# Optimization experiments

Hardware: AMD Instinct MI355X
Metric: run time of the kernel (lower is better)

## Reference

```python
import jax, jax.numpy as jnp
import numpy as np

D_MODEL = 256
N_LAYERS = 4
D_STATE = 16
D_CONV = 4
D_INNER = 2 * D_MODEL          # expand=2
DT_RANK = (D_MODEL + 15) // 16  # 'auto' -> ceil(d_model/16) = 16
NUM_CLASSES = 10
BATCH = 4
HW = 32


def setup_inputs() -> dict:
    key = jax.random.key(0)
    ks = jax.random.split(key, 16)
    std = 0.02
    inp = {}
    inp["x"] = jax.random.normal(ks[0], (BATCH, 3, HW, HW), dtype=jnp.float32)
    inp["input_proj_w"] = std * jax.random.normal(ks[1], (D_MODEL, 3), dtype=jnp.float32)
    inp["input_proj_b"] = jnp.zeros((D_MODEL,), jnp.float32)
    inp["in_proj_w"] = std * jax.random.normal(ks[2], (N_LAYERS, 2 * D_INNER, D_MODEL), dtype=jnp.float32)
    inp["conv_w"] = std * jax.random.normal(ks[3], (N_LAYERS, D_INNER, D_CONV), dtype=jnp.float32)
    inp["conv_b"] = jnp.zeros((N_LAYERS, D_INNER), jnp.float32)
    inp["x_proj_w"] = std * jax.random.normal(ks[4], (N_LAYERS, DT_RANK + 2 * D_STATE, D_INNER), dtype=jnp.float32)
    inp["dt_proj_w"] = std * jax.random.normal(ks[5], (N_LAYERS, D_INNER, DT_RANK), dtype=jnp.float32)
    # dt bias ~ inverse-softplus of small dt values (Mamba-style init)
    inp["dt_proj_b"] = jnp.log(jnp.expm1(0.01 * jnp.ones((N_LAYERS, D_INNER), jnp.float32)))
    # A_log init: log(1..d_state) per channel (Mamba S4D-real init)
    a = jnp.log(jnp.arange(1, D_STATE + 1, dtype=jnp.float32))
    inp["A_log"] = jnp.broadcast_to(a, (N_LAYERS, D_INNER, D_STATE)).copy()
    inp["D_skip"] = jnp.ones((N_LAYERS, D_INNER), jnp.float32)
    inp["out_proj_w"] = std * jax.random.normal(ks[6], (N_LAYERS, D_MODEL, D_INNER), dtype=jnp.float32)
    inp["ln_w"] = jnp.ones((N_LAYERS, D_MODEL), jnp.float32)
    inp["ln_b"] = jnp.zeros((N_LAYERS, D_MODEL), jnp.float32)
    inp["fn_w"] = jnp.ones((D_MODEL,), jnp.float32)
    inp["fn_b"] = jnp.zeros((D_MODEL,), jnp.float32)
    inp["cls_w"] = std * jax.random.normal(ks[7], (NUM_CLASSES, D_MODEL), dtype=jnp.float32)
    inp["cls_b"] = jnp.zeros((NUM_CLASSES,), jnp.float32)
    return inp


def _layer_norm(x, w, b, eps=1e-5):
    mu = jnp.mean(x, axis=-1, keepdims=True)
    var = jnp.mean(jnp.square(x - mu), axis=-1, keepdims=True)
    return (x - mu) * jax.lax.rsqrt(var + eps) * w + b


def _mamba_block(x, in_w, cw, cb, xp_w, dt_w, dt_b, A_log, D_skip, out_w):
    B_, L, _ = x.shape
    xz = jnp.einsum('bld,ed->ble', x, in_w)            # [B,L,2*Din]
    xh, z = jnp.split(xz, 2, axis=-1)                  # [B,L,Din] each
    # depthwise causal conv1d (kernel D_CONV, left pad D_CONV-1)
    xp = jnp.pad(xh, ((0, 0), (D_CONV - 1, 0), (0, 0)))
    conv = cb + sum(xp[:, k:k + L, :] * cw[:, k] for k in range(D_CONV))
    xh = jax.nn.silu(conv)
    x_dbl = jnp.einsum('bld,ed->ble', xh, xp_w)        # [B,L,dt_rank+2N]
    dt, Bm, Cm = jnp.split(x_dbl, [DT_RANK, DT_RANK + D_STATE], axis=-1)
    delta = jax.nn.softplus(jnp.einsum('blr,dr->bld', dt, dt_w) + dt_b)  # [B,L,Din]
    A = -jnp.exp(A_log)                                # [Din,N]
    deltaA = jnp.exp(delta[..., None] * A)             # [B,L,Din,N]
    deltaBu = delta[..., None] * Bm[:, :, None, :] * xh[..., None]       # [B,L,Din,N]

    def step(h, inputs):
        dA_t, dBu_t, C_t = inputs
        h = dA_t * h + dBu_t                           # [B,Din,N]
        y = jnp.einsum('bdn,bn->bd', h, C_t)
        return h, y

    h0 = jnp.zeros((B_, D_INNER, D_STATE), x.dtype)
    _, ys = jax.lax.scan(step, h0, (deltaA.transpose(1, 0, 2, 3),
                                    deltaBu.transpose(1, 0, 2, 3),
                                    Cm.transpose(1, 0, 2)))
    y = ys.transpose(1, 0, 2) + xh * D_skip            # [B,L,Din]
    y = y * jax.nn.silu(z)
    return jnp.einsum('bld,od->blo', y, out_w)         # [B,L,Dmodel]


def reference(x, input_proj_w, input_proj_b, in_proj_w, conv_w, conv_b,
              x_proj_w, dt_proj_w, dt_proj_b, A_log, D_skip, out_proj_w,
              ln_w, ln_b, fn_w, fn_b, cls_w, cls_b):
    B_ = x.shape[0]
    seq = x.transpose(0, 2, 3, 1).reshape(B_, -1, 3)   # [B, H*W, 3]
    h = jnp.einsum('blc,dc->bld', seq, input_proj_w) + input_proj_b
    for i in range(N_LAYERS):
        res = h
        h = _layer_norm(h, ln_w[i], ln_b[i])
        h = _mamba_block(h, in_proj_w[i], conv_w[i], conv_b[i], x_proj_w[i],
                         dt_proj_w[i], dt_proj_b[i], A_log[i], D_skip[i], out_proj_w[i])
        h = h + res  # dropout is identity (p=0 / eval)
    h = jnp.mean(h, axis=1)                            # [B, Dmodel]
    h = _layer_norm(h, fn_w, fn_b)
    return h @ cls_w.T + cls_b                         # [B, num_classes]
```

## Files before the change

kernel.cpp:

```cpp
#include <hip/hip_runtime.h>
#include <math.h>

#define B_ 4
#define L_ 1024
#define DM 256
#define DIN 512
#define NST 16
#define DTR 16
#define CHK 64
#define CT (L_ / CHK)

typedef short short8 __attribute__((ext_vector_type(8)));
typedef float float4v __attribute__((ext_vector_type(4)));

__device__ __forceinline__ float softplusf(float x) {
    return (x > 20.f) ? x : log1pf(__expf(x));
}
__device__ __forceinline__ float siluf(float x) {
    return x / (1.f + __expf(-x));
}
__device__ __forceinline__ unsigned short f2bf(float f) {
    unsigned int u = __float_as_uint(f);
    u = (u + 0x7fffu + ((u >> 16) & 1u)) >> 16;
    return (unsigned short)u;
}

__device__ __forceinline__ void block_reduce2(float& a, float& q) {
    #pragma unroll
    for (int off = 32; off > 0; off >>= 1) {
        a += __shfl_down(a, off);
        q += __shfl_down(q, off);
    }
    __shared__ float sa[4], sq[4];
    int lane = threadIdx.x & 63, w = threadIdx.x >> 6;
    if (lane == 0) { sa[w] = a; sq[w] = q; }
    __syncthreads();
    a = sa[0] + sa[1] + sa[2] + sa[3];
    q = sq[0] + sq[1] + sq[2] + sq[3];
}

__global__ __launch_bounds__(256) void prologue_kernel(
    const float* __restrict__ inw, int na, const float* __restrict__ xpw, int nb,
    const float* __restrict__ opw, int nc,
    unsigned short* __restrict__ oa, unsigned short* __restrict__ ob,
    unsigned short* __restrict__ oc, int nconv,
    const float* __restrict__ x, const float* __restrict__ ipw,
    const float* __restrict__ ipb, const float* __restrict__ lw0,
    const float* __restrict__ lb0, float* __restrict__ h0,
    unsigned short* __restrict__ ln16)
{
    if ((int)blockIdx.x < nconv) {
        int i = blockIdx.x * 256 + threadIdx.x;
        if (i < na) { oa[i] = f2bf(inw[i]); return; }
        int j = i - na;
        if (j < nb) { ob[j] = f2bf(xpw[j]); return; }
        int k = j - nb;
        if (k < nc) oc[k] = f2bf(opw[k]);
        return;
    }
    int row = blockIdx.x - nconv;
    int l = row & (L_ - 1);
    int b = row >> 10;
    int d = threadIdx.x;
    const float* xb = x + (size_t)b * 3 * L_;
    float x0 = xb[l], x1 = xb[L_ + l], x2 = xb[2 * L_ + l];
    float acc = ipb[d];
    acc = fmaf(x0, ipw[d * 3 + 0], acc);
    acc = fmaf(x1, ipw[d * 3 + 1], acc);
    acc = fmaf(x2, ipw[d * 3 + 2], acc);
    float a = acc, q = acc * acc;
    block_reduce2(a, q);
    float mu = a * (1.f / DM);
    float var = q * (1.f / DM) - mu * mu;
    float rs = rsqrtf(var + 1e-5f);
    h0[(size_t)row * DM + d] = acc;
    ln16[(size_t)row * DM + d] = f2bf((acc - mu) * rs * lw0[d] + lb0[d]);
}

__global__ __launch_bounds__(256) void gemm_bt_bf16(
    const unsigned short* __restrict__ A, const unsigned short* __restrict__ W,
    float* __restrict__ C, int M, int N, int K, int lda)
{
    __shared__ unsigned short As[64][72];
    __shared__ unsigned short Ws[64][72];
    const int tid = threadIdx.x;
    const int wave = tid >> 6;
    const int lane = tid & 63;
    const int m_l = lane & 15;
    const int q = lane >> 4;
    const int m0 = blockIdx.y * 64;
    const int n0 = blockIdx.x * 64;
    const int sr = tid >> 3;
    const int sc = (tid & 7) * 8;

    float4v acc[4];
    #pragma unroll
    for (int j = 0; j < 4; ++j) acc[j] = (float4v)(0.f);

    for (int k0 = 0; k0 < K; k0 += 64) {
        *(short8*)&As[sr][sc]      = *(const short8*)(A + (size_t)(m0 + sr) * lda + k0 + sc);
        *(short8*)&As[sr + 32][sc] = *(const short8*)(A + (size_t)(m0 + sr + 32) * lda + k0 + sc);
        *(short8*)&Ws[sr][sc]      = *(const short8*)(W + (size_t)(n0 + sr) * K + k0 + sc);
        *(short8*)&Ws[sr + 32][sc] = *(const short8*)(W + (size_t)(n0 + sr + 32) * K + k0 + sc);
        __syncthreads();
        #pragma unroll
        for (int kk = 0; kk < 64; kk += 32) {
            short8 a = *(const short8*)&As[wave * 16 + m_l][kk + q * 8];
            #pragma unroll
            for (int j4 = 0; j4 < 4; ++j4) {
                short8 bf = *(const short8*)&Ws[j4 * 16 + m_l][kk + q * 8];
                acc[j4] = __builtin_amdgcn_mfma_f32_16x16x32_bf16(a, bf, acc[j4], 0, 0, 0);
            }
        }
        __syncthreads();
    }
    #pragma unroll
    for (int j4 = 0; j4 < 4; ++j4) {
        int n = n0 + j4 * 16 + m_l;
        #pragma unroll
        for (int reg = 0; reg < 4; ++reg) {
            int m = m0 + wave * 16 + q * 4 + reg;
            C[(size_t)m * N + n] = acc[j4][reg];
        }
    }
}

__global__ __launch_bounds__(512) void conv_xproj_summary(
    const float* __restrict__ xz, const float* __restrict__ cw,
    const float* __restrict__ cb, const unsigned short* __restrict__ W,
    const float* __restrict__ A_log, const float* __restrict__ dt_w,
    const float* __restrict__ dt_b,
    float* __restrict__ dbc, float* __restrict__ S, float* __restrict__ H)
{
    __shared__ unsigned short As[CT][520];
    __shared__ float Dbc[CT][64];
    const int tid = threadIdx.x;
    const int d = tid;
    const int c = blockIdx.x;
    const int b = blockIdx.y;
    const int l0 = c * CT;

    float xcr[CT];
    {
        const float w0 = cw[d * 4 + 0], w1 = cw[d * 4 + 1];
        const float w2 = cw[d * 4 + 2], w3 = cw[d * 4 + 3];
        const float cbv = cb[d];
        const float* xp = xz + ((size_t)(b * L_ + l0)) * (2 * DIN) + d;
        float x0 = 0.f, x1 = 0.f, x2 = 0.f;
        if (l0 >= 3) {
            x0 = xp[(ptrdiff_t)(-3) * (2 * DIN)];
            x1 = xp[(ptrdiff_t)(-2) * (2 * DIN)];
            x2 = xp[(ptrdiff_t)(-1) * (2 * DIN)];
        }
        #pragma unroll
        for (int t = 0; t < CT; ++t) {
            float x3 = xp[(size_t)t * (2 * DIN)];
            float a = fmaf(x0, w0, cbv);
            a = fmaf(x1, w1, a);
            a = fmaf(x2, w2, a);
            a = fmaf(x3, w3, a);
            float v = siluf(a);
            xcr[t] = v;
            As[t][d] = f2bf(v);
            x0 = x1; x1 = x2; x2 = x3;
        }
    }
    __syncthreads();

    {
        const int wave = tid >> 6;
        const int lane = tid & 63;
        const int m_l = lane & 15;
        const int q = lane >> 4;
        if (wave < 3) {
            float4v acc = (float4v)(0.f);
            for (int k0 = 0; k0 < DIN; k0 += 32) {
                short8 a  = *(const short8*)&As[m_l][k0 + q * 8];
                short8 bf = *(const short8*)(W + (size_t)(wave * 16 + m_l) * DIN + k0 + q * 8);
                acc = __builtin_amdgcn_mfma_f32_16x16x32_bf16(a, bf, acc, 0, 0, 0);
            }
            #pragma unroll
            for (int reg = 0; reg < 4; ++reg)
                Dbc[q * 4 + reg][wave * 16 + m_l] = acc[reg];
        }
    }
    __syncthreads();

    for (int i = tid; i < CT * 48; i += 512) {
        int t = i / 48, col = i - t * 48;
        dbc[((size_t)(b * L_ + l0 + t)) * 48 + col] = Dbc[t][col];
    }

    float A[NST], tw[DTR];
    #pragma unroll
    for (int j = 0; j < NST; ++j) A[j] = -__expf(A_log[d * NST + j]);
    #pragma unroll
    for (int r = 0; r < DTR; ++r) tw[r] = dt_w[d * DTR + r];
    const float tb = dt_b[d];
    float h[NST];
    #pragma unroll
    for (int j = 0; j < NST; ++j) h[j] = 0.f;
    float ssum = 0.f;
    #pragma unroll 4
    for (int t = 0; t < CT; ++t) {
        float acc = tb;
        #pragma unroll
        for (int r = 0; r < DTR; ++r) acc = fmaf(Dbc[t][r], tw[r], acc);
        float dlt = softplusf(acc);
        float t0 = dlt * xcr[t];
        ssum += dlt;
        #pragma unroll
        for (int j = 0; j < NST; ++j) {
            float dA = __expf(A[j] * dlt);
            h[j] = fmaf(dA, h[j], t0 * Dbc[t][DTR + j]);
        }
    }
    S[((size_t)b * CHK + c) * DIN + d] = ssum;
    float* Hp = H + (((size_t)b * CHK + c) * NST) * DIN + d;
    #pragma unroll
    for (int j = 0; j < NST; ++j)
        Hp[(size_t)j * DIN] = h[j];
}

__global__ __launch_bounds__(256) void scan_prefix_kernel(
    const float* __restrict__ S, float* __restrict__ H,
    const float* __restrict__ A_log)
{
    int idx = blockIdx.x * 256 + threadIdx.x;
    int d = idx & (DIN - 1);
    int n = (idx >> 9) & (NST - 1);
    int b = idx >> 13;
    float A = -__expf(A_log[d * NST + n]);
    float hprev = 0.f;
    const float* Sp = S + (size_t)b * CHK * DIN + d;
    float* Hp = H + (((size_t)b * CHK) * NST + n) * DIN + d;
    for (int c = 0; c < CHK; ++c) {
        float Hc = Hp[(size_t)c * NST * DIN];
        float Sc = Sp[(size_t)c * DIN];
        Hp[(size_t)c * NST * DIN] = hprev;
        hprev = fmaf(__expf(A * Sc), hprev, Hc);
    }
}

__global__ __launch_bounds__(512) void scan_apply_out(
    const float* __restrict__ dbc, const float* __restrict__ xz,
    const float* __restrict__ cw, const float* __restrict__ cb,
    const float* __restrict__ A_log, const float* __restrict__ dt_w,
    const float* __restrict__ dt_b, const float* __restrict__ Dskip,
    const float* __restrict__ H, const unsigned short* __restrict__ Wout,
    float* __restrict__ hbuf, const float* __restrict__ nlw,
    const float* __restrict__ nlb, unsigned short* __restrict__ ln16,
    float* __restrict__ chunkpartial, int last)
{
    __shared__ unsigned short Ys[CT][520];
    __shared__ float hrow[CT][264];
    const int tid = threadIdx.x;
    const int d = tid;
    const int c = blockIdx.x;
    const int b = blockIdx.y;
    const int l0 = c * CT;

    {
        float A[NST], tw[DTR];
        #pragma unroll
        for (int j = 0; j < NST; ++j) A[j] = -__expf(A_log[d * NST + j]);
        #pragma unroll
        for (int r = 0; r < DTR; ++r) tw[r] = dt_w[d * DTR + r];
        const float tb = dt_b[d];
        const float Dsk = Dskip[d];
        const float* bc = dbc + ((size_t)(b * L_ + l0)) * 48;
        const float* xp = xz  + ((size_t)(b * L_ + l0)) * (2 * DIN) + d;
        const float* zp = xp + DIN;

        const float w0 = cw[d * 4 + 0], w1 = cw[d * 4 + 1];
        const float w2 = cw[d * 4 + 2], w3 = cw[d * 4 + 3];
        const float cbv = cb[d];
        float x0 = 0.f, x1 = 0.f, x2 = 0.f;
        if (l0 >= 3) {
            x0 = xp[(ptrdiff_t)(-3) * (2 * DIN)];
            x1 = xp[(ptrdiff_t)(-2) * (2 * DIN)];
            x2 = xp[(ptrdiff_t)(-1) * (2 * DIN)];
        }

        float h[NST];
        const float* Hp = H + (((size_t)b * CHK + c) * NST) * DIN + d;
        #pragma unroll
        for (int j = 0; j < NST; ++j) h[j] = Hp[(size_t)j * DIN];

        #pragma unroll 4
        for (int t = 0; t < CT; ++t) {
            float x3 = xp[(size_t)t * (2 * DIN)];
            float ca = fmaf(x0, w0, cbv);
            ca = fmaf(x1, w1, ca);
            ca = fmaf(x2, w2, ca);
            ca = fmaf(x3, w3, ca);
            float xcv = siluf(ca);
            x0 = x1; x1 = x2; x2 = x3;

            const float* br = bc + t * 48;
            float acc = tb;
            #pragma unroll
            for (int r = 0; r < DTR; ++r) acc = fmaf(br[r], tw[r], acc);
            float dlt = softplusf(acc);
            float zv  = zp[(size_t)t * (2 * DIN)];
            float t0 = dlt * xcv;
            float p = 0.f;
            #pragma unroll
            for (int j = 0; j < NST; ++j) {
                float dA = __expf(A[j] * dlt);
                h[j] = fmaf(dA, h[j], t0 * br[DTR + j]);
                p = fmaf(h[j], br[DTR + NST + j], p);
            }
            Ys[t][d] = f2bf((p + xcv * Dsk) * siluf(zv));
        }
    }
    __syncthreads();

    {
        const int row = tid >> 5;
        const int col0 = (tid & 31) * 8;
        const float* hg = hbuf + ((size_t)(b * L_ + l0 + row)) * DM + col0;
        *(float4*)&hrow[row][col0]     = *(const float4*)hg;
        *(float4*)&hrow[row][col0 + 4] = *(const float4*)(hg + 4);
    }
    __syncthreads();

    {
        const int wave = tid >> 6;
        const int lane = tid & 63;
        const int m_l = lane & 15;
        const int q = lane >> 4;
        #pragma unroll
        for (int nt = 0; nt < 2; ++nt) {
            const int n0 = (wave * 2 + nt) * 16;
            float4v acc;
            #pragma unroll
            for (int reg = 0; reg < 4; ++reg)
                acc[reg] = hrow[q * 4 + reg][n0 + m_l];
            for (int k0 = 0; k0 < DIN; k0 += 32) {
                short8 a = *(const short8*)&Ys[m_l][k0 + q * 8];
                short8 w = *(const short8*)(Wout + (size_t)(n0 + m_l) * DIN + k0 + q * 8);
                acc = __builtin_amdgcn_mfma_f32_16x16x32_bf16(a, w, acc, 0, 0, 0);
            }
            #pragma unroll
            for (int reg = 0; reg < 4; ++reg)
                hrow[q * 4 + reg][n0 + m_l] = acc[reg];
        }
    }
    __syncthreads();

    if (!last) {
        const int row = tid >> 5;
        const int c32 = tid & 31;
        const int col0 = c32 * 8;
        float v[8];
        float s = 0.f, qq = 0.f;
        #pragma unroll
        for (int i = 0; i < 8; ++i) {
            v[i] = hrow[row][col0 + i];
            s += v[i];
            qq += v[i] * v[i];
        }
        s += __shfl_xor(s, 1);  qq += __shfl_xor(qq, 1);
        s += __shfl_xor(s, 2);  qq += __shfl_xor(qq, 2);
        s += __shfl_xor(s, 4);  qq += __shfl_xor(qq, 4);
        s += __shfl_xor(s, 8);  qq += __shfl_xor(qq, 8);
        s += __shfl_xor(s, 16); qq += __shfl_xor(qq, 16);
        float mu = s * (1.f / DM);
        float var = qq * (1.f / DM) - mu * mu;
        float rs = rsqrtf(var + 1e-5f);
        float* hg = hbuf + ((size_t)(b * L_ + l0 + row)) * DM + col0;
        *(float4*)hg       = make_float4(v[0], v[1], v[2], v[3]);
        *(float4*)(hg + 4) = make_float4(v[4], v[5], v[6], v[7]);
        unsigned short* lo = ln16 + ((size_t)(b * L_ + l0 + row)) * DM + col0;
        #pragma unroll
        for (int i = 0; i < 8; ++i)
            lo[i] = f2bf((v[i] - mu) * rs * nlw[col0 + i] + nlb[col0 + i]);
    } else {
        if (tid < DM) {
            float s = 0.f;
            #pragma unroll
            for (int t = 0; t < CT; ++t) s += hrow[t][tid];
            chunkpartial[((size_t)(b * CHK + c)) * DM + tid] = s;
        }
    }
}

__global__ __launch_bounds__(256) void head_final_kernel(
    const float* __restrict__ chunkpartial, const float* __restrict__ fn_w,
    const float* __restrict__ fn_b, const float* __restrict__ cls_w,
    const float* __restrict__ cls_b, float* __restrict__ out)
{
    int b = blockIdx.x, t = threadIdx.x;
    const float* pp = chunkpartial + (size_t)b * CHK * DM + t;
    float s = 0.f;
    #pragma unroll 8
    for (int c = 0; c < CHK; ++c) s += pp[(size_t)c * DM];
    s *= (1.f / L_);
    float a = s, q = s * s;
    block_reduce2(a, q);
    float mu = a * (1.f / DM);
    float var = q * (1.f / DM) - mu * mu;
    float v = (s - mu) * rsqrtf(var + 1e-5f) * fn_w[t] + fn_b[t];
    __shared__ float pooled[DM];
    pooled[t] = v;
    __syncthreads();
    if (t < 10) {
        float acc = cls_b[t];
        for (int d2 = 0; d2 < DM; ++d2)
            acc = fmaf(pooled[d2], cls_w[t * DM + d2], acc);
        out[b * 10 + t] = acc;
    }
}

extern "C" void kernel_launch(void* const* d_in, const int* in_sizes, int n_in,
                              void* d_out, int out_size, void* d_ws, size_t ws_size,
                              hipStream_t stream)
{
    const float* x    = (const float*)d_in[0];
    const float* ipw  = (const float*)d_in[1];
    const float* ipb  = (const float*)d_in[2];
    const float* inw  = (const float*)d_in[3];
    const float* cw   = (const float*)d_in[4];
    const float* cb   = (const float*)d_in[5];
    const float* xpw  = (const float*)d_in[6];
    const float* dtw  = (const float*)d_in[7];
    const float* dtb  = (const float*)d_in[8];
    const float* alog = (const float*)d_in[9];
    const float* dsk  = (const float*)d_in[10];
    const float* opw  = (const float*)d_in[11];
    const float* lnw  = (const float*)d_in[12];
    const float* lnb  = (const float*)d_in[13];
    const float* fnw  = (const float*)d_in[14];
    const float* fnb  = (const float*)d_in[15];
    const float* clw  = (const float*)d_in[16];
    const float* clb  = (const float*)d_in[17];

    float* ws     = (float*)d_ws;
    float* hbuf   = ws;
    float* xzbuf  = hbuf   + (size_t)B_ * L_ * DM;
    float* dbcbuf = xzbuf  + (size_t)B_ * L_ * 2 * DIN;
    float* Sbuf   = dbcbuf + (size_t)B_ * L_ * 48;
    float* Hbuf   = Sbuf   + (size_t)B_ * CHK * DIN;
    float* cpart  = Hbuf   + (size_t)B_ * CHK * NST * DIN;
    float* tail   = cpart  + (size_t)B_ * CHK * DM;
    unsigned short* ln16  = (unsigned short*)tail;
    unsigned short* inw16 = ln16  + (size_t)B_ * L_ * DM;
    unsigned short* xpw16 = inw16 + (size_t)4 * 1024 * DM;
    unsigned short* opw16 = xpw16 + (size_t)4 * 48 * DIN;

    const int BL = B_ * L_;
    const int NIN = 4 * 1024 * DM, NXP = 4 * 48 * DIN, NOP = 4 * DM * DIN;
    const int NCONV = (NIN + NXP + NOP + 255) / 256;

    prologue_kernel<<<NCONV + BL, 256, 0, stream>>>(
        inw, NIN, xpw, NXP, opw, NOP, inw16, xpw16, opw16, NCONV,
        x, ipw, ipb, lnw, lnb, hbuf, ln16);

    for (int i = 0; i < 4; ++i) {
        gemm_bt_bf16<<<dim3(2 * DIN / 64, BL / 64), 256, 0, stream>>>(
            ln16, inw16 + (size_t)i * 1024 * DM, xzbuf, BL, 2 * DIN, DM, DM);
        conv_xproj_summary<<<dim3(CHK, B_), 512, 0, stream>>>(
            xzbuf, cw + i * DIN * 4, cb + i * DIN,
            xpw16 + (size_t)i * 48 * DIN, alog + i * DIN * NST,
            dtw + i * DIN * DTR, dtb + i * DIN, dbcbuf, Sbuf, Hbuf);
        scan_prefix_kernel<<<B_ * NST * DIN / 256, 256, 0, stream>>>(
            Sbuf, Hbuf, alog + i * DIN * NST);
        int last = (i == 3);
        const float* nlw = lnw + (last ? 0 : (i + 1) * DM);
        const float* nlb = lnb + (last ? 0 : (i + 1) * DM);
        scan_apply_out<<<dim3(CHK, B_), 512, 0, stream>>>(
            dbcbuf, xzbuf, cw + i * DIN * 4, cb + i * DIN,
            alog + i * DIN * NST, dtw + i * DIN * DTR, dtb + i * DIN,
            dsk + i * DIN, Hbuf, opw16 + (size_t)i * DM * DIN, hbuf,
            nlw, nlb, ln16, cpart, last);
    }

    head_final_kernel<<<B_, 256, 0, stream>>>(cpart, fnw, fnb, clw, clb,
                                              (float*)d_out);
}
```

Baseline: 385.6 us.

## Fuse in_proj GEMM into conv/xproj kernel and inline chunk-prefix scan into apply

The standalone in_proj GEMM is folded into a per-chunk front kernel. Each block computes its 19-row (16 plus 3 halo) slice of xz via MFMA, keeps the x half in shared memory for the causal conv, and writes conv output and z to separate buffers. The separate scan_prefix kernel is removed: each back-kernel block recomputes its incoming state by looping over all preceding chunk summaries. The change cuts two launches per layer and the xz round trip through memory. In exchange it recomputes halo rows in the GEMM, re-reads in_proj weights from global in every block, and gives later chunks up to 63 serial prefix steps of 16 exps each.

```diff
diff --git a/kernel.cpp b/kernel.cpp
--- a/kernel.cpp
+++ b/kernel.cpp
@@ -77,84 +77,82 @@
     ln16[(size_t)row * DM + d] = f2bf((acc - mu) * rs * lw0[d] + lb0[d]);
 }
 
-__global__ __launch_bounds__(256) void gemm_bt_bf16(
-    const unsigned short* __restrict__ A, const unsigned short* __restrict__ W,
-    float* __restrict__ C, int M, int N, int K, int lda)
+__global__ __launch_bounds__(512) void layer_front(
+    const unsigned short* __restrict__ ln16, const unsigned short* __restrict__ Win,
+    const float* __restrict__ cw, const float* __restrict__ cb,
+    const unsigned short* __restrict__ Wxp, const float* __restrict__ A_log,
+    const float* __restrict__ dt_w, const float* __restrict__ dt_b,
+    float* __restrict__ xcbuf, float* __restrict__ zbuf,
+    float* __restrict__ dbc, float* __restrict__ S, float* __restrict__ H)
 {
-    __shared__ unsigned short As[64][72];
-    __shared__ unsigned short Ws[64][72];
+    __shared__ unsigned short UN[8448];
+    __shared__ float xh[19][528];
+    __shared__ float Dbc[CT][64];
+    unsigned short (*Ln)[264] = (unsigned short (*)[264])UN;
+    unsigned short (*As)[520] = (unsigned short (*)[520])UN;
+
     const int tid = threadIdx.x;
+    const int c = blockIdx.x;
+    const int b = blockIdx.y;
+    const int l0 = c * CT;
     const int wave = tid >> 6;
     const int lane = tid & 63;
     const int m_l = lane & 15;
     const int q = lane >> 4;
-    const int m0 = blockIdx.y * 64;
-    const int n0 = blockIdx.x * 64;
-    const int sr = tid >> 3;
-    const int sc = (tid & 7) * 8;
-
-    float4v acc[4];
-    #pragma unroll
-    for (int j = 0; j < 4; ++j) acc[j] = (float4v)(0.f);
-
-    for (int k0 = 0; k0 < K; k0 += 64) {
-        *(short8*)&As[sr][sc]      = *(const short8*)(A + (size_t)(m0 + sr) * lda + k0 + sc);
-        *(short8*)&As[sr + 32][sc] = *(const short8*)(A + (size_t)(m0 + sr + 32) * lda + k0 + sc);
-        *(short8*)&Ws[sr][sc]      = *(const short8*)(W + (size_t)(n0 + sr) * K + k0 + sc);
-        *(short8*)&Ws[sr + 32][sc] = *(const short8*)(W + (size_t)(n0 + sr + 32) * K + k0 + sc);
-        __syncthreads();
-        #pragma unroll
-        for (int kk = 0; kk < 64; kk += 32) {
-            short8 a = *(const short8*)&As[wave * 16 + m_l][kk + q * 8];
-            #pragma unroll
-            for (int j4 = 0; j4 < 4; ++j4) {
-                short8 bf = *(const short8*)&Ws[j4 * 16 + m_l][kk + q * 8];
-                acc[j4] = __builtin_amdgcn_mfma_f32_16x16x32_bf16(a, bf, acc[j4], 0, 0, 0);
+
+    {
+        const int sr = tid >> 5;
+        const int sc = (tid & 31) * 8;
+        #pragma unroll
+        for (int p = 0; p < 2; ++p) {
+            int row = sr + p * 16;
+            int rr = row > 18 ? 18 : row;
+            int gl = l0 - 3 + rr;
+            if (gl < 0) gl = 0;
+            *(short8*)&Ln[row][sc] =
+                *(const short8*)(ln16 + ((size_t)(b * L_ + gl)) * DM + sc);
+        }
+    }
+    __syncthreads();
+
+    #pragma unroll
+    for (int mt = 0; mt < 2; ++mt) {
+        #pragma unroll
+        for (int nt = 0; nt < 8; ++nt) {
+            const int n0 = wave * 128 + nt * 16;
+            float4v acc = (float4v)(0.f);
+            for (int k0 = 0; k0 < DM; k0 += 32) {
+                short8 a = *(const short8*)&Ln[mt * 16 + m_l][k0 + q * 8];
+                short8 w = *(const short8*)(Win + (size_t)(n0 + m_l) * DM + k0 + q * 8);
+                acc = __builtin_amdgcn_mfma_f32_16x16x32_bf16(a, w, acc, 0, 0, 0);
             }
-        }
-        __syncthreads();
-    }
-    #pragma unroll
-    for (int j4 = 0; j4 < 4; ++j4) {
-        int n = n0 + j4 * 16 + m_l;
-        #pragma unroll
-        for (int reg = 0; reg < 4; ++reg) {
-            int m = m0 + wave * 16 + q * 4 + reg;
-            C[(size_t)m * N + n] = acc[j4][reg];
-        }
-    }
-}
-
-__global__ __launch_bounds__(512) void conv_xproj_summary(
-    const float* __restrict__ xz, const float* __restrict__ cw,
-    const float* __restrict__ cb, const unsigned short* __restrict__ W,
-    const float* __restrict__ A_log, const float* __restrict__ dt_w,
-    const float* __restrict__ dt_b,
-    float* __restrict__ dbc, float* __restrict__ S, float* __restrict__ H)
-{
-    __shared__ unsigned short As[CT][520];
-    __shared__ float Dbc[CT][64];
-    const int tid = threadIdx.x;
+            const int col = n0 + m_l;
+            #pragma unroll
+            for (int reg = 0; reg < 4; ++reg) {
+                int r = mt * 16 + q * 4 + reg;
+                if (r < 19) {
+                    if (col < DIN)
+                        xh[r][col] = acc[reg];
+                    else if (r >= 3)
+                        zbuf[((size_t)(b * L_ + l0 + r - 3)) * DIN + (col - DIN)] = acc[reg];
+                }
+            }
+        }
+    }
+    __syncthreads();
+
     const int d = tid;
-    const int c = blockIdx.x;
-    const int b = blockIdx.y;
-    const int l0 = c * CT;
-
+    if (c == 0) { xh[0][d] = 0.f; xh[1][d] = 0.f; xh[2][d] = 0.f; }
     float xcr[CT];
     {
         const float w0 = cw[d * 4 + 0], w1 = cw[d * 4 + 1];
         const float w2 = cw[d * 4 + 2], w3 = cw[d * 4 + 3];
         const float cbv = cb[d];
-        const float* xp = xz + ((size_t)(b * L_ + l0)) * (2 * DIN) + d;
-        float x0 = 0.f, x1 = 0.f, x2 = 0.f;
-        if (l0 >= 3) {
-            x0 = xp[(ptrdiff_t)(-3) * (2 * DIN)];
-            x1 = xp[(ptrdiff_t)(-2) * (2 * DIN)];
-            x2 = xp[(ptrdiff_t)(-1) * (2 * DIN)];
-        }
+        float x0 = xh[0][d], x1 = xh[1][d], x2 = xh[2][d];
+        float* xcg = xcbuf + ((size_t)(b * L_ + l0)) * DIN + d;
         #pragma unroll
         for (int t = 0; t < CT; ++t) {
-            float x3 = xp[(size_t)t * (2 * DIN)];
+            float x3 = xh[t + 3][d];
             float a = fmaf(x0, w0, cbv);
             a = fmaf(x1, w1, a);
             a = fmaf(x2, w2, a);
@@ -162,27 +160,22 @@
             float v = siluf(a);
             xcr[t] = v;
             As[t][d] = f2bf(v);
+            xcg[(size_t)t * DIN] = v;
             x0 = x1; x1 = x2; x2 = x3;
         }
     }
     __syncthreads();
 
-    {
-        const int wave = tid >> 6;
-        const int lane = tid & 63;
-        const int m_l = lane & 15;
-        const int q = lane >> 4;
-        if (wave < 3) {
-            float4v acc = (float4v)(0.f);
-            for (int k0 = 0; k0 < DIN; k0 += 32) {
-                short8 a  = *(const short8*)&As[m_l][k0 + q * 8];
-                short8 bf = *(const short8*)(W + (size_t)(wave * 16 + m_l) * DIN + k0 + q * 8);
-                acc = __builtin_amdgcn_mfma_f32_16x16x32_bf16(a, bf, acc, 0, 0, 0);
-            }
-            #pragma unroll
-            for (int reg = 0; reg < 4; ++reg)
-                Dbc[q * 4 + reg][wave * 16 + m_l] = acc[reg];
-        }
+    if (wave < 3) {
+        float4v acc = (float4v)(0.f);
+        for (int k0 = 0; k0 < DIN; k0 += 32) {
+            short8 a  = *(const short8*)&As[m_l][k0 + q * 8];
+            short8 bf = *(const short8*)(Wxp + (size_t)(wave * 16 + m_l) * DIN + k0 + q * 8);
+            acc = __builtin_amdgcn_mfma_f32_16x16x32_bf16(a, bf, acc, 0, 0, 0);
+        }
+        #pragma unroll
+        for (int reg = 0; reg < 4; ++reg)
+            Dbc[q * 4 + reg][wave * 16 + m_l] = acc[reg];
     }
     __syncthreads();
 
@@ -222,31 +215,11 @@
         Hp[(size_t)j * DIN] = h[j];
 }
 
-__global__ __launch_bounds__(256) void scan_prefix_kernel(
-    const float* __restrict__ S, float* __restrict__ H,
-    const float* __restrict__ A_log)
-{
-    int idx = blockIdx.x * 256 + threadIdx.x;
-    int d = idx & (DIN - 1);
-    int n = (idx >> 9) & (NST - 1);
-    int b = idx >> 13;
-    float A = -__expf(A_log[d * NST + n]);
-    float hprev = 0.f;
-    const float* Sp = S + (size_t)b * CHK * DIN + d;
-    float* Hp = H + (((size_t)b * CHK) * NST + n) * DIN + d;
-    for (int c = 0; c < CHK; ++c) {
-        float Hc = Hp[(size_t)c * NST * DIN];
-        float Sc = Sp[(size_t)c * DIN];
-        Hp[(size_t)c * NST * DIN] = hprev;
-        hprev = fmaf(__expf(A * Sc), hprev, Hc);
-    }
-}
-
-__global__ __launch_bounds__(512) void scan_apply_out(
-    const float* __restrict__ dbc, const float* __restrict__ xz,
-    const float* __restrict__ cw, const float* __restrict__ cb,
-    const float* __restrict__ A_log, const float* __restrict__ dt_w,
-    const float* __restrict__ dt_b, const float* __restrict__ Dskip,
+__global__ __launch_bounds__(512) void layer_back(
+    const float* __restrict__ dbc, const float* __restrict__ xcbuf,
+    const float* __restrict__ zbuf, const float* __restrict__ A_log,
+    const float* __restrict__ dt_w, const float* __restrict__ dt_b,
+    const float* __restrict__ Dskip, const float* __restrict__ S,
     const float* __restrict__ H, const unsigned short* __restrict__ Wout,
     float* __restrict__ hbuf, const float* __restrict__ nlw,
     const float* __restrict__ nlb, unsigned short* __restrict__ ln16,
@@ -268,41 +241,34 @@
         for (int r = 0; r < DTR; ++r) tw[r] = dt_w[d * DTR + r];
         const float tb = dt_b[d];
         const float Dsk = Dskip[d];
-        const float* bc = dbc + ((size_t)(b * L_ + l0)) * 48;
-        const float* xp = xz  + ((size_t)(b * L_ + l0)) * (2 * DIN) + d;
-        const float* zp = xp + DIN;
-
-        const float w0 = cw[d * 4 + 0], w1 = cw[d * 4 + 1];
-        const float w2 = cw[d * 4 + 2], w3 = cw[d * 4 + 3];
-        const float cbv = cb[d];
-        float x0 = 0.f, x1 = 0.f, x2 = 0.f;
-        if (l0 >= 3) {
-            x0 = xp[(ptrdiff_t)(-3) * (2 * DIN)];
-            x1 = xp[(ptrdiff_t)(-2) * (2 * DIN)];
-            x2 = xp[(ptrdiff_t)(-1) * (2 * DIN)];
-        }
+        const float* bc = dbc   + ((size_t)(b * L_ + l0)) * 48;
+        const float* xp = xcbuf + ((size_t)(b * L_ + l0)) * DIN + d;
+        const float* zp = zbuf  + ((size_t)(b * L_ + l0)) * DIN + d;
 
         float h[NST];
-        const float* Hp = H + (((size_t)b * CHK + c) * NST) * DIN + d;
-        #pragma unroll
-        for (int j = 0; j < NST; ++j) h[j] = Hp[(size_t)j * DIN];
+        #pragma unroll
+        for (int j = 0; j < NST; ++j) h[j] = 0.f;
+        {
+            const float* Sp = S + (size_t)b * CHK * DIN + d;
+            const float* Hp = H + ((size_t)b * CHK * NST) * DIN + d;
+            for (int cc = 0; cc < c; ++cc) {
+                float Sc = Sp[(size_t)cc * DIN];
+                const float* Hc = Hp + ((size_t)cc * NST) * DIN;
+                #pragma unroll
+                for (int j = 0; j < NST; ++j)
+                    h[j] = fmaf(__expf(A[j] * Sc), h[j], Hc[(size_t)j * DIN]);
+            }
+        }
 
         #pragma unroll 4
         for (int t = 0; t < CT; ++t) {
-            float x3 = xp[(size_t)t * (2 * DIN)];
-            float ca = fmaf(x0, w0, cbv);
-            ca = fmaf(x1, w1, ca);
-            ca = fmaf(x2, w2, ca);
-            ca = fmaf(x3, w3, ca);
-            float xcv = siluf(ca);
-            x0 = x1; x1 = x2; x2 = x3;
-
             const float* br = bc + t * 48;
             float acc = tb;
             #pragma unroll
             for (int r = 0; r < DTR; ++r) acc = fmaf(br[r], tw[r], acc);
             float dlt = softplusf(acc);
-            float zv  = zp[(size_t)t * (2 * DIN)];
+            float xcv = xp[(size_t)t * DIN];
+            float zv  = zp[(size_t)t * DIN];
             float t0 = dlt * xcv;
             float p = 0.f;
             #pragma unroll
@@ -351,8 +317,7 @@
 
     if (!last) {
         const int row = tid >> 5;
-        const int c32 = tid & 31;
-        const int col0 = c32 * 8;
+        const int col0 = (tid & 31) * 8;
         float v[8];
         float s = 0.f, qq = 0.f;
         #pragma unroll
@@ -438,8 +403,9 @@
 
     float* ws     = (float*)d_ws;
     float* hbuf   = ws;
-    float* xzbuf  = hbuf   + (size_t)B_ * L_ * DM;
-    float* dbcbuf = xzbuf  + (size_t)B_ * L_ * 2 * DIN;
+    float* xcbuf  = hbuf   + (size_t)B_ * L_ * DM;
+    float* zbuf   = xcbuf  + (size_t)B_ * L_ * DIN;
+    float* dbcbuf = zbuf   + (size_t)B_ * L_ * DIN;
     float* Sbuf   = dbcbuf + (size_t)B_ * L_ * 48;
     float* Hbuf   = Sbuf   + (size_t)B_ * CHK * DIN;
     float* cpart  = Hbuf   + (size_t)B_ * CHK * NST * DIN;
@@ -458,21 +424,19 @@
         x, ipw, ipb, lnw, lnb, hbuf, ln16);
 
     for (int i = 0; i < 4; ++i) {
-        gemm_bt_bf16<<<dim3(2 * DIN / 64, BL / 64), 256, 0, stream>>>(
-            ln16, inw16 + (size_t)i * 1024 * DM, xzbuf, BL, 2 * DIN, DM, DM);
-        conv_xproj_summary<<<dim3(CHK, B_), 512, 0, stream>>>(
-            xzbuf, cw + i * DIN * 4, cb + i * DIN,
+        layer_front<<<dim3(CHK, B_), 512, 0, stream>>>(
+            ln16, inw16 + (size_t)i * 1024 * DM,
+            cw + i * DIN * 4, cb + i * DIN,
             xpw16 + (size_t)i * 48 * DIN, alog + i * DIN * NST,
-            dtw + i * DIN * DTR, dtb + i * DIN, dbcbuf, Sbuf, Hbuf);
-        scan_prefix_kernel<<<B_ * NST * DIN / 256, 256, 0, stream>>>(
-            Sbuf, Hbuf, alog + i * DIN * NST);
+            dtw + i * DIN * DTR, dtb + i * DIN,
+            xcbuf, zbuf, dbcbuf, Sbuf, Hbuf);
         int last = (i == 3);
         const float* nlw = lnw + (last ? 0 : (i + 1) * DM);
         const float* nlb = lnb + (last ? 0 : (i + 1) * DM);
-        scan_apply_out<<<dim3(CHK, B_), 512, 0, stream>>>(
-            dbcbuf, xzbuf, cw + i * DIN * 4, cb + i * DIN,
-            alog + i * DIN * NST, dtw + i * DIN * DTR, dtb + i * DIN,
-            dsk + i * DIN, Hbuf, opw16 + (size_t)i * DM * DIN, hbuf,
+        layer_back<<<dim3(CHK, B_), 512, 0, stream>>>(
+            dbcbuf, xcbuf, zbuf, alog + i * DIN * NST,
+            dtw + i * DIN * DTR, dtb + i * DIN, dsk + i * DIN,
+            Sbuf, Hbuf, opw16 + (size_t)i * DM * DIN, hbuf,
             nlw, nlb, ln16, cpart, last);
     }
 
```

New measurement: 494.9 us. 1.28x slower.
